# Kernel optimization log

Hardware: AMD Instinct MI355X
Metric: run time of the kernel (lower is better)

Reference implementation:

```python
import jax, jax.numpy as jnp
import numpy as np

B, T, D = 16, 512, 512
MEL_MAX = 4096


def setup_inputs() -> dict:
    key = jax.random.key(0)
    k0, k1, k2, k3 = jax.random.split(key, 4)
    x = jax.random.normal(k0, (B, T, D), dtype=jnp.float32)
    # integer frame durations per phoneme (the `target` used in training-mode LR)
    target = jax.random.randint(k1, (B, T), 0, 8, dtype=jnp.int32)
    scale = 1.0 / np.sqrt(D)
    W1 = jax.random.normal(k2, (D, D), dtype=jnp.float32) * scale
    b1 = jnp.zeros((D,), dtype=jnp.float32)
    W2 = jax.random.normal(k3, (D, 1), dtype=jnp.float32) * scale
    b2 = jnp.zeros((1,), dtype=jnp.float32)
    return {"x": x, "W1": W1, "b1": b1, "W2": W2, "b2": b2,
            "target": target, "mel_max_length": MEL_MAX}


def _length_regulate(x, durations, mel_max_length):
    """Vectorized repeat_interleave + pad.
    x: [B,T,D] float, durations: [B,T] int, output: [B,mel_max_length,D].
    Equivalent to per-batch torch expand+cat then pad, done via cumsum+searchsorted gather.
    """
    cs = jnp.cumsum(durations, axis=1)                    # [B,T] exclusive upper bounds
    pos = jnp.arange(mel_max_length)                      # [L]

    def expand_one(xb, csb):
        idx = jnp.searchsorted(csb, pos, side='right')    # [L] phoneme index per frame
        valid = pos < csb[-1]                             # frames beyond total -> pad
        idx = jnp.clip(idx, 0, xb.shape[0] - 1)
        return jnp.where(valid[:, None], xb[idx], jnp.zeros((), xb.dtype))

    return jax.vmap(expand_one)(x, cs)                    # [B,L,D]


def reference(x, W1, b1, W2, b2, target, mel_max_length):
    # DurationPredictor: Linear(512,512)+ReLU, Linear(512,1)+ReLU, squeeze -> [B,T]
    h = jax.nn.relu(jnp.einsum('btd,de->bte', x, W1) + b1)
    duration_predictor_output = jax.nn.relu(jnp.einsum('bte,eo->bto', h, W2) + b2)[..., 0]
    # Training-mode LR: expand x by integer `target` durations, pad to mel_max_length
    output = _length_regulate(x, target, mel_max_length)
    return output, duration_predictor_output
```

## Files before the change

### kernel.cpp

```cpp
#include <hip/hip_runtime.h>
#include <hip/hip_bf16.h>

#define BSZ 16
#define TT 512
#define DD 512
#define MM (BSZ * TT)
#define NPART 16
#define NMEGA 1024

typedef __attribute__((ext_vector_type(8))) short bf16x8;
typedef __attribute__((ext_vector_type(8))) unsigned short ushort8;
typedef __attribute__((ext_vector_type(4))) float f32x4;

__global__ __launch_bounds__(256) void prep_kernel(const float* __restrict__ W1,
                                                   const int* __restrict__ target,
                                                   ushort* __restrict__ wth,
                                                   int* __restrict__ imap, int L) {
    int bid = blockIdx.x;
    if (bid < 256) {
        int t = bid * 256 + threadIdx.x;
        int n  = t & (DD - 1);
        int kq = t >> 9;
        ushort hh[4];
        #pragma unroll
        for (int i = 0; i < 4; ++i) {
            float f = W1[(size_t)(kq * 4 + i) * DD + n];
            __hip_bfloat16 bh = __float2bfloat16(f);
            hh[i] = *(ushort*)&bh;
        }
        ((ushort4*)wth)[(size_t)n * (DD / 4) + kq] = make_ushort4(hh[0], hh[1], hh[2], hh[3]);
    } else {
        int b = bid - 256;
        __shared__ int s[TT];
        int t = threadIdx.x;
        s[t]       = target[b * TT + t];
        s[t + 256] = target[b * TT + t + 256];
        __syncthreads();
        #pragma unroll
        for (int off = 1; off < TT; off <<= 1) {
            int v0 = (t >= off) ? s[t - off] : 0;
            int v1 = s[t + 256 - off];
            __syncthreads();
            s[t] += v0;
            s[t + 256] += v1;
            __syncthreads();
        }
        int total = s[TT - 1];
        int* imb = imap + (size_t)b * L;
        for (int ph = t; ph < TT; ph += 256) {
            int st = (ph == 0) ? 0 : s[ph - 1];
            int en = s[ph];
            for (int d = st; d < en; ++d) imb[d] = ph;
        }
        for (int l = total + t; l < L; l += 256) imb[l] = -1;
    }
}

#define BM 64
#define BN 64
#define BK 64
__global__ __launch_bounds__(256, 4) void mega_kernel(const ushort* __restrict__ wth,
                                                      const float* __restrict__ b1,
                                                      const float* __restrict__ W2,
                                                      const float* __restrict__ x,
                                                      const int* __restrict__ imap,
                                                      float* __restrict__ out,
                                                      float* __restrict__ partial,
                                                      int L) {
    __shared__ ushort ldsA[2][BM * 64];
    __shared__ ushort ldsB[2][BN * 64];
    const int bid = blockIdx.x;
    const int t = threadIdx.x;
    const int lane = t & 63, wave = t >> 6;
    const int rt = bid >> 3, ct = bid & 7;
    const int row0 = rt * BM, col0 = ct * BN;
    const int rq = t >> 3;
    const int ls = (t & 7) ^ (rq & 7);
    const int sco = ls * 8;
    const int ar = t >> 2;
    const int ac = (t & 3) * 16;

    const int b_lr   = bid >> 6;
    const int chunk0 = (bid & 63) * 64;

    auto do_lr = [&]() {
        const f32x4* x4g = (const f32x4*)(x + (size_t)b_lr * TT * DD);
        f32x4*       o4  = (f32x4*)(out + (size_t)b_lr * L * DD);
        const int*   imb = imap + (size_t)b_lr * L;
        const int lr_lane = t & 127;
        const int lr_half = t >> 7;
        #pragma unroll
        for (int c = 0; c < 4; ++c) {
            int rb = chunk0 + c * 16 + lr_half;
            int idxs[8];
            #pragma unroll
            for (int p = 0; p < 8; ++p) idxs[p] = imb[rb + p * 2];
            f32x4 gv[8];
            #pragma unroll
            for (int p = 0; p < 8; ++p)
                gv[p] = (idxs[p] >= 0) ? x4g[(size_t)idxs[p] * (DD / 4) + lr_lane]
                                       : (f32x4){0.f, 0.f, 0.f, 0.f};
            #pragma unroll
            for (int p = 0; p < 8; ++p)
                __builtin_nontemporal_store(gv[p], &o4[(size_t)(rb + p * 2) * (DD / 4) + lr_lane]);
        }
    };

    auto stageB = [&](int buf, int kt) {
        const int k0 = kt * BK;
        #pragma unroll
        for (int q = 0; q < 2; ++q) {
            int row = q * 32 + rq;
            const ushort* gb = wth + (size_t)(col0 + row) * DD + k0 + sco;
            auto lb = (__attribute__((address_space(3))) unsigned int*)
                      ((char*)&ldsB[buf][0] + q * 4096 + wave * 1024);
            __builtin_amdgcn_global_load_lds(
                (const __attribute__((address_space(1))) unsigned int*)gb, lb, 16, 0, 0);
        }
    };
    auto stageA = [&](int buf, int kt) {
        const float* xa = x + (size_t)(row0 + ar) * DD + kt * BK + ac;
        float fl[16];
        *(f32x4*)&fl[0]  = ((const f32x4*)xa)[0];
        *(f32x4*)&fl[4]  = ((const f32x4*)xa)[1];
        *(f32x4*)&fl[8]  = ((const f32x4*)xa)[2];
        *(f32x4*)&fl[12] = ((const f32x4*)xa)[3];
        ushort us[16];
        #pragma unroll
        for (int j = 0; j < 16; ++j) {
            __hip_bfloat16 bh = __float2bfloat16(fl[j]);
            us[j] = *(ushort*)&bh;
        }
        int s0 = ((t & 3) * 2)     ^ (ar & 7);
        int s1 = ((t & 3) * 2 + 1) ^ (ar & 7);
        *(ushort8*)&ldsA[buf][ar * 64 + s0 * 8] = *(ushort8*)&us[0];
        *(ushort8*)&ldsA[buf][ar * 64 + s1 * 8] = *(ushort8*)&us[8];
    };

    auto do_gemm = [&]() {
        const int wm = (wave >> 1) * 32;
        const int wn = (wave & 1) * 32;
        const int l15 = lane & 15, l4 = lane >> 4;
        f32x4 acc[2][2] = {};

        stageB(0, 0);
        stageA(0, 0);
        __syncthreads();
        int cur = 0;
        #pragma unroll 1
        for (int kt = 0; kt < DD / BK; ++kt) {
            if (kt + 1 < DD / BK) {
                stageB(cur ^ 1, kt + 1);
                stageA(cur ^ 1, kt + 1);
            }
            const ushort* At = &ldsA[cur][0];
            const ushort* Bt = &ldsB[cur][0];
            bf16x8 a[2][2], b[2][2];
            #pragma unroll
            for (int i = 0; i < 2; ++i) {
                int r = wm + i * 16 + l15;
                #pragma unroll
                for (int ks = 0; ks < 2; ++ks) {
                    int sl = (ks * 4 + l4) ^ (r & 7);
                    a[i][ks] = *(const bf16x8*)&At[r * 64 + sl * 8];
                }
            }
            #pragma unroll
            for (int j = 0; j < 2; ++j) {
                int r = wn + j * 16 + l15;
                #pragma unroll
                for (int ks = 0; ks < 2; ++ks) {
                    int sl = (ks * 4 + l4) ^ (r & 7);
                    b[j][ks] = *(const bf16x8*)&Bt[r * 64 + sl * 8];
                }
            }
            #pragma unroll
            for (int ks = 0; ks < 2; ++ks)
                #pragma unroll
                for (int i = 0; i < 2; ++i)
                    #pragma unroll
                    for (int j = 0; j < 2; ++j)
                        acc[i][j] = __builtin_amdgcn_mfma_f32_16x16x32_bf16(a[i][ks], b[j][ks], acc[i][j], 0, 0, 0);
            __syncthreads();
            cur ^= 1;
        }

        const int pslice = ct * 2 + (wn >> 5);
        #pragma unroll
        for (int i = 0; i < 2; ++i) {
            #pragma unroll
            for (int r = 0; r < 4; ++r) {
                float s = 0.f;
                #pragma unroll
                for (int j = 0; j < 2; ++j) {
                    int cg = col0 + wn + j * 16 + l15;
                    float h = acc[i][j][r] + b1[cg];
                    h = fmaxf(h, 0.f);
                    s += h * W2[cg];
                }
                s += __shfl_xor(s, 1);
                s += __shfl_xor(s, 2);
                s += __shfl_xor(s, 4);
                s += __shfl_xor(s, 8);
                if (l15 == 0) {
                    int rg = row0 + wm + i * 16 + l4 * 4 + r;
                    partial[(size_t)pslice * MM + rg] = s;
                }
            }
        }
    };

    if (bid & 1) { do_lr(); do_gemm(); }
    else         { do_gemm(); do_lr(); }
}

__global__ __launch_bounds__(256) void dpo_kernel(const float* __restrict__ partial,
                                                  const float* __restrict__ b2,
                                                  float* __restrict__ dpo) {
    int m = blockIdx.x * 256 + threadIdx.x;
    float s = b2[0];
    #pragma unroll
    for (int nb = 0; nb < NPART; ++nb) s += partial[(size_t)nb * MM + m];
    dpo[m] = fmaxf(s, 0.f);
}

extern "C" void kernel_launch(void* const* d_in, const int* in_sizes, int n_in,
                              void* d_out, int out_size, void* d_ws, size_t ws_size,
                              hipStream_t stream) {
    const float* x      = (const float*)d_in[0];
    const float* W1     = (const float*)d_in[1];
    const float* b1     = (const float*)d_in[2];
    const float* W2     = (const float*)d_in[3];
    const float* b2     = (const float*)d_in[4];
    const int*   target = (const int*)d_in[5];
    int L = (out_size - BSZ * TT) / (BSZ * DD);

    float* out_lr  = (float*)d_out;
    float* out_dpo = (float*)d_out + (size_t)BSZ * L * DD;

    ushort* wth     = (ushort*)d_ws;
    float*  partial = (float*)(wth + (size_t)DD * DD);
    int*    imap    = (int*)(partial + (size_t)NPART * MM);

    prep_kernel<<<dim3(272), dim3(256), 0, stream>>>(W1, target, wth, imap, L);
    mega_kernel<<<dim3(NMEGA), dim3(256), 0, stream>>>(wth, b1, W2, x, imap,
                                                       out_lr, partial, L);
    dpo_kernel<<<dim3(MM / 256), dim3(256), 0, stream>>>(partial, b2, out_dpo);
}
```

Measured before the change: 51.89 us.

## Split mega kernel blocks into separate GEMM and length-regulate roles

The grid doubles so each block does either the length-regulate gather or one GEMM tile, where before every block did both in alternating order. The GEMM now uses a single LDS buffer instead of double buffering, which halves shared memory per block but removes the overlap of global loads with MFMA work. The gather's nontemporal stores become plain stores. The aim is better load balance and occupancy between the memory-bound copy and the compute, at the cost of an exposed load latency on each K step.

After: 50.87 us. -2.0%, faster.

```diff
diff --git a/kernel.cpp b/kernel.cpp
--- a/kernel.cpp
+++ b/kernel.cpp
@@ -6,7 +6,7 @@
 #define DD 512
 #define MM (BSZ * TT)
 #define NPART 16
-#define NMEGA 1024
+#define NMEGA 2048
 
 typedef __attribute__((ext_vector_type(8))) short bf16x8;
 typedef __attribute__((ext_vector_type(8))) unsigned short ushort8;
@@ -56,9 +56,6 @@
     }
 }
 
-#define BM 64
-#define BN 64
-#define BK 64
 __global__ __launch_bounds__(256, 4) void mega_kernel(const ushort* __restrict__ wth,
                                                       const float* __restrict__ b1,
                                                       const float* __restrict__ W2,
@@ -67,151 +64,135 @@
                                                       float* __restrict__ out,
                                                       float* __restrict__ partial,
                                                       int L) {
-    __shared__ ushort ldsA[2][BM * 64];
-    __shared__ ushort ldsB[2][BN * 64];
+    __shared__ ushort ldsA[64 * 64];
+    __shared__ ushort ldsB[64 * 64];
     const int bid = blockIdx.x;
     const int t = threadIdx.x;
     const int lane = t & 63, wave = t >> 6;
-    const int rt = bid >> 3, ct = bid & 7;
-    const int row0 = rt * BM, col0 = ct * BN;
+    const int role = (bid >> 3) & 1;
+    const int id = (bid >> 4) * 8 + (bid & 7);
+
+    if (role == 1) {
+        const int b_lr   = id >> 6;
+        const int chunk0 = (id & 63) * 64;
+        const f32x4* x4g = (const f32x4*)(x + (size_t)b_lr * TT * DD);
+        f32x4*       o4  = (f32x4*)(out + (size_t)b_lr * L * DD);
+        const int*   imb = imap + (size_t)b_lr * L;
+        const int lr_lane = t & 127;
+        const int lr_half = t >> 7;
+        #pragma unroll
+        for (int c = 0; c < 4; ++c) {
+            const int rb = chunk0 + c * 16 + lr_half;
+            int idxs[8];
+            #pragma unroll
+            for (int p = 0; p < 8; ++p) idxs[p] = imb[rb + p * 2];
+            f32x4 gv[8];
+            #pragma unroll
+            for (int p = 0; p < 8; ++p)
+                gv[p] = (idxs[p] >= 0) ? x4g[(size_t)idxs[p] * (DD / 4) + lr_lane]
+                                       : (f32x4){0.f, 0.f, 0.f, 0.f};
+            #pragma unroll
+            for (int p = 0; p < 8; ++p)
+                o4[(size_t)(rb + p * 2) * (DD / 4) + lr_lane] = gv[p];
+        }
+        return;
+    }
+
+    const int row0 = (id >> 3) * 64;
+    const int col0 = (id & 7) * 64;
     const int rq = t >> 3;
     const int ls = (t & 7) ^ (rq & 7);
     const int sco = ls * 8;
     const int ar = t >> 2;
     const int ac = (t & 3) * 16;
-
-    const int b_lr   = bid >> 6;
-    const int chunk0 = (bid & 63) * 64;
-
-    auto do_lr = [&]() {
-        const f32x4* x4g = (const f32x4*)(x + (size_t)b_lr * TT * DD);
-        f32x4*       o4  = (f32x4*)(out + (size_t)b_lr * L * DD);
-        const int*   imb = imap + (size_t)b_lr * L;
-        const int lr_lane = t & 127;
-        const int lr_half = t >> 7;
-        #pragma unroll
-        for (int c = 0; c < 4; ++c) {
-            int rb = chunk0 + c * 16 + lr_half;
-            int idxs[8];
-            #pragma unroll
-            for (int p = 0; p < 8; ++p) idxs[p] = imb[rb + p * 2];
-            f32x4 gv[8];
-            #pragma unroll
-            for (int p = 0; p < 8; ++p)
-                gv[p] = (idxs[p] >= 0) ? x4g[(size_t)idxs[p] * (DD / 4) + lr_lane]
-                                       : (f32x4){0.f, 0.f, 0.f, 0.f};
-            #pragma unroll
-            for (int p = 0; p < 8; ++p)
-                __builtin_nontemporal_store(gv[p], &o4[(size_t)(rb + p * 2) * (DD / 4) + lr_lane]);
-        }
-    };
-
-    auto stageB = [&](int buf, int kt) {
-        const int k0 = kt * BK;
+    const int wm = (wave >> 1) * 32;
+    const int wn = (wave & 1) * 32;
+    const int l15 = lane & 15, l4 = lane >> 4;
+    f32x4 acc[2][2] = {};
+
+    #pragma unroll 1
+    for (int kt = 0; kt < DD / 64; ++kt) {
+        const int k0 = kt * 64;
         #pragma unroll
         for (int q = 0; q < 2; ++q) {
             int row = q * 32 + rq;
             const ushort* gb = wth + (size_t)(col0 + row) * DD + k0 + sco;
             auto lb = (__attribute__((address_space(3))) unsigned int*)
-                      ((char*)&ldsB[buf][0] + q * 4096 + wave * 1024);
+                      ((char*)&ldsB[0] + q * 4096 + wave * 1024);
             __builtin_amdgcn_global_load_lds(
                 (const __attribute__((address_space(1))) unsigned int*)gb, lb, 16, 0, 0);
         }
-    };
-    auto stageA = [&](int buf, int kt) {
-        const float* xa = x + (size_t)(row0 + ar) * DD + kt * BK + ac;
-        float fl[16];
-        *(f32x4*)&fl[0]  = ((const f32x4*)xa)[0];
-        *(f32x4*)&fl[4]  = ((const f32x4*)xa)[1];
-        *(f32x4*)&fl[8]  = ((const f32x4*)xa)[2];
-        *(f32x4*)&fl[12] = ((const f32x4*)xa)[3];
-        ushort us[16];
-        #pragma unroll
-        for (int j = 0; j < 16; ++j) {
-            __hip_bfloat16 bh = __float2bfloat16(fl[j]);
-            us[j] = *(ushort*)&bh;
-        }
-        int s0 = ((t & 3) * 2)     ^ (ar & 7);
-        int s1 = ((t & 3) * 2 + 1) ^ (ar & 7);
-        *(ushort8*)&ldsA[buf][ar * 64 + s0 * 8] = *(ushort8*)&us[0];
-        *(ushort8*)&ldsA[buf][ar * 64 + s1 * 8] = *(ushort8*)&us[8];
-    };
-
-    auto do_gemm = [&]() {
-        const int wm = (wave >> 1) * 32;
-        const int wn = (wave & 1) * 32;
-        const int l15 = lane & 15, l4 = lane >> 4;
-        f32x4 acc[2][2] = {};
-
-        stageB(0, 0);
-        stageA(0, 0);
+        {
+            const float* xa = x + (size_t)(row0 + ar) * DD + k0 + ac;
+            float fl[16];
+            *(f32x4*)&fl[0]  = ((const f32x4*)xa)[0];
+            *(f32x4*)&fl[4]  = ((const f32x4*)xa)[1];
+            *(f32x4*)&fl[8]  = ((const f32x4*)xa)[2];
+            *(f32x4*)&fl[12] = ((const f32x4*)xa)[3];
+            ushort us[16];
+            #pragma unroll
+            for (int j = 0; j < 16; ++j) {
+                __hip_bfloat16 bh = __float2bfloat16(fl[j]);
+                us[j] = *(ushort*)&bh;
+            }
+            int s0 = ((t & 3) * 2)     ^ (ar & 7);
+            int s1 = ((t & 3) * 2 + 1) ^ (ar & 7);
+            *(ushort8*)&ldsA[ar * 64 + s0 * 8] = *(ushort8*)&us[0];
+            *(ushort8*)&ldsA[ar * 64 + s1 * 8] = *(ushort8*)&us[8];
+        }
         __syncthreads();
-        int cur = 0;
-        #pragma unroll 1
-        for (int kt = 0; kt < DD / BK; ++kt) {
-            if (kt + 1 < DD / BK) {
-                stageB(cur ^ 1, kt + 1);
-                stageA(cur ^ 1, kt + 1);
-            }
-            const ushort* At = &ldsA[cur][0];
-            const ushort* Bt = &ldsB[cur][0];
-            bf16x8 a[2][2], b[2][2];
-            #pragma unroll
-            for (int i = 0; i < 2; ++i) {
-                int r = wm + i * 16 + l15;
+        bf16x8 a[2][2], b[2][2];
+        #pragma unroll
+        for (int i = 0; i < 2; ++i) {
+            int r = wm + i * 16 + l15;
+            #pragma unroll
+            for (int ks = 0; ks < 2; ++ks) {
+                int sl = (ks * 4 + l4) ^ (r & 7);
+                a[i][ks] = *(const bf16x8*)&ldsA[r * 64 + sl * 8];
+            }
+        }
+        #pragma unroll
+        for (int j = 0; j < 2; ++j) {
+            int r = wn + j * 16 + l15;
+            #pragma unroll
+            for (int ks = 0; ks < 2; ++ks) {
+                int sl = (ks * 4 + l4) ^ (r & 7);
+                b[j][ks] = *(const bf16x8*)&ldsB[r * 64 + sl * 8];
+            }
+        }
+        #pragma unroll
+        for (int ks = 0; ks < 2; ++ks)
+            #pragma unroll
+            for (int i = 0; i < 2; ++i)
                 #pragma unroll
-                for (int ks = 0; ks < 2; ++ks) {
-                    int sl = (ks * 4 + l4) ^ (r & 7);
-                    a[i][ks] = *(const bf16x8*)&At[r * 64 + sl * 8];
-                }
-            }
+                for (int j = 0; j < 2; ++j)
+                    acc[i][j] = __builtin_amdgcn_mfma_f32_16x16x32_bf16(a[i][ks], b[j][ks], acc[i][j], 0, 0, 0);
+        __syncthreads();
+    }
+
+    const int pslice = (id & 7) * 2 + (wn >> 5);
+    #pragma unroll
+    for (int i = 0; i < 2; ++i) {
+        #pragma unroll
+        for (int r = 0; r < 4; ++r) {
+            float s = 0.f;
             #pragma unroll
             for (int j = 0; j < 2; ++j) {
-                int r = wn + j * 16 + l15;
-                #pragma unroll
-                for (int ks = 0; ks < 2; ++ks) {
-                    int sl = (ks * 4 + l4) ^ (r & 7);
-                    b[j][ks] = *(const bf16x8*)&Bt[r * 64 + sl * 8];
-                }
-            }
-            #pragma unroll
-            for (int ks = 0; ks < 2; ++ks)
-                #pragma unroll
-                for (int i = 0; i < 2; ++i)
-                    #pragma unroll
-                    for (int j = 0; j < 2; ++j)
-                        acc[i][j] = __builtin_amdgcn_mfma_f32_16x16x32_bf16(a[i][ks], b[j][ks], acc[i][j], 0, 0, 0);
-            __syncthreads();
-            cur ^= 1;
-        }
-
-        const int pslice = ct * 2 + (wn >> 5);
-        #pragma unroll
-        for (int i = 0; i < 2; ++i) {
-            #pragma unroll
-            for (int r = 0; r < 4; ++r) {
-                float s = 0.f;
-                #pragma unroll
-                for (int j = 0; j < 2; ++j) {
-                    int cg = col0 + wn + j * 16 + l15;
-                    float h = acc[i][j][r] + b1[cg];
-                    h = fmaxf(h, 0.f);
-                    s += h * W2[cg];
-                }
-                s += __shfl_xor(s, 1);
-                s += __shfl_xor(s, 2);
-                s += __shfl_xor(s, 4);
-                s += __shfl_xor(s, 8);
-                if (l15 == 0) {
-                    int rg = row0 + wm + i * 16 + l4 * 4 + r;
-                    partial[(size_t)pslice * MM + rg] = s;
-                }
-            }
-        }
-    };
-
-    if (bid & 1) { do_lr(); do_gemm(); }
-    else         { do_gemm(); do_lr(); }
+                int cg = col0 + wn + j * 16 + l15;
+                float h = acc[i][j][r] + b1[cg];
+                h = fmaxf(h, 0.f);
+                s += h * W2[cg];
+            }
+            s += __shfl_xor(s, 1);
+            s += __shfl_xor(s, 2);
+            s += __shfl_xor(s, 4);
+            s += __shfl_xor(s, 8);
+            if (l15 == 0) {
+                int rg = row0 + wm + i * 16 + l4 * 4 + r;
+                partial[(size_t)pslice * MM + rg] = s;
+            }
+        }
+    }
 }
 
 __global__ __launch_bounds__(256) void dpo_kernel(const float* __restrict__ partial,
```
